# Optimization experiments

Measured on AMD Instinct MI355X. Metric: run time of the kernel, lower is better.

Reference implementation:

```python
import jax, jax.numpy as jnp
import numpy as np

N_NODES = 50000
N_EDGES = 800000


def setup_inputs() -> dict:
    key = jax.random.key(0)
    ks = jax.random.split(key, 8)
    return {
        "x": jax.random.normal(ks[0], (N_NODES, 256), dtype=jnp.float32),
        "adj_vals": jax.random.uniform(ks[1], (N_EDGES,), dtype=jnp.float32),
        "rows": jax.random.randint(ks[2], (N_EDGES,), 0, N_NODES, dtype=jnp.int32),
        "cols": jax.random.randint(ks[3], (N_EDGES,), 0, N_NODES, dtype=jnp.int32),
        "W1": jax.random.normal(ks[4], (256, 256), dtype=jnp.float32) * (1.0 / np.sqrt(256)),
        "b1": jnp.zeros((256,), dtype=jnp.float32),
        "W2": jax.random.normal(ks[5], (256, 256), dtype=jnp.float32) * (1.0 / np.sqrt(256)),
        "b2": jnp.zeros((256,), dtype=jnp.float32),
        "W3": jax.random.normal(ks[6], (256, 128), dtype=jnp.float32) * (1.0 / np.sqrt(256)),
        "b3": jnp.zeros((128,), dtype=jnp.float32),
    }


def reference(x, adj_vals, rows, cols, W1, b1, W2, b2, W3, b3):
    n = x.shape[0]

    def spmm(h):
        # sparse adjacency matmul: out[r] += val * h[c] over all edges (r, c)
        return jax.ops.segment_sum(adj_vals[:, None] * h[cols], rows, num_segments=n)

    # GCNLayer: adj @ (x @ W) + b ; ReLU between layers (dropout p=0 => identity)
    h = jax.nn.relu(spmm(x @ W1) + b1)
    h = jax.nn.relu(spmm(h @ W2) + b2)
    return spmm(h @ W3) + b3
```

## Files before the change

kernel.cpp:

```cpp
#include <hip/hip_runtime.h>
#include <hip/hip_bf16.h>


#define N_NODES 50000
#define N_EDGES 800000
#define KDIM 256
#define REP 8
#define NC (N_NODES * REP)
#define NB2 ((NC + 1023) / 1024)
#define NC_PAD (NB2 * 1024)

typedef __attribute__((ext_vector_type(8))) short short8;
typedef __attribute__((ext_vector_type(4))) float f32x4;

__device__ __forceinline__ ushort f2bf(float f) {
    union { float f; unsigned u; } x; x.f = f;
    unsigned r = x.u + 0x7fffu + ((x.u >> 16) & 1u);
    return (ushort)(r >> 16);
}
__device__ __forceinline__ float bf2f(ushort u) {
    union { unsigned u; float f; } x; x.u = ((unsigned)u) << 16;
    return x.f;
}

__global__ __launch_bounds__(256) void transpose_all_kernel(
        const float* __restrict__ W1, const float* __restrict__ W2,
        const float* __restrict__ W3, ushort* __restrict__ Wt1,
        ushort* __restrict__ Wt2, ushort* __restrict__ Wt3) {
    int id = blockIdx.x * blockDim.x + threadIdx.x;
    if (id < 65536) {
        int n = id >> 8, k = id & 255;
        Wt1[n * 256 + k] = f2bf(W1[k * 256 + n]);
    } else if (id < 131072) {
        int i = id - 65536, n = i >> 8, k = i & 255;
        Wt2[n * 256 + k] = f2bf(W2[k * 256 + n]);
    } else if (id < 163840) {
        int i = id - 131072, n = i >> 8, k = i & 255;
        Wt3[n * 256 + k] = f2bf(W3[k * 128 + n]);
    }
}


#define LDK 40

template <bool AFP32>
__device__ __forceinline__ void gemm_body(
        const void* __restrict__ Ain, const ushort* __restrict__ Wt,
        ushort* __restrict__ C, int M, int N, int bx, int by) {
    __shared__ ushort As[128 * LDK];
    __shared__ ushort Ws[128 * LDK];

    int t = threadIdx.x;
    int lane = t & 63;
    int w = t >> 6;
    int row0 = bx * 128, col0 = by * 128;
    int wm = (w & 1) * 64, wn = (w >> 1) * 64;
    int q = lane >> 4, mi = lane & 15;
    int r0 = t >> 2, kc = (t & 3) * 8;

    f32x4 acc[4][4];
    #pragma unroll
    for (int i = 0; i < 4; i++)
        #pragma unroll
        for (int j = 0; j < 4; j++) acc[i][j] = (f32x4)0.f;

    for (int k0 = 0; k0 < KDIM; k0 += 32) {
        int ga0 = row0 + r0;       if (ga0 >= M) ga0 = M - 1;
        int ga1 = row0 + r0 + 64;  if (ga1 >= M) ga1 = M - 1;
        short8 a0, a1;
        if (AFP32) {
            const float* Af = (const float*)Ain;
            float4 f0 = *(const float4*)&Af[ga0 * KDIM + k0 + kc];
            float4 f1 = *(const float4*)&Af[ga0 * KDIM + k0 + kc + 4];
            float4 f2 = *(const float4*)&Af[ga1 * KDIM + k0 + kc];
            float4 f3 = *(const float4*)&Af[ga1 * KDIM + k0 + kc + 4];
            a0[0] = (short)f2bf(f0.x); a0[1] = (short)f2bf(f0.y);
            a0[2] = (short)f2bf(f0.z); a0[3] = (short)f2bf(f0.w);
            a0[4] = (short)f2bf(f1.x); a0[5] = (short)f2bf(f1.y);
            a0[6] = (short)f2bf(f1.z); a0[7] = (short)f2bf(f1.w);
            a1[0] = (short)f2bf(f2.x); a1[1] = (short)f2bf(f2.y);
            a1[2] = (short)f2bf(f2.z); a1[3] = (short)f2bf(f2.w);
            a1[4] = (short)f2bf(f3.x); a1[5] = (short)f2bf(f3.y);
            a1[6] = (short)f2bf(f3.z); a1[7] = (short)f2bf(f3.w);
        } else {
            const ushort* Ab = (const ushort*)Ain;
            a0 = *(const short8*)&Ab[ga0 * KDIM + k0 + kc];
            a1 = *(const short8*)&Ab[ga1 * KDIM + k0 + kc];
        }
        short8 b0 = *(const short8*)&Wt[(col0 + r0) * KDIM + k0 + kc];
        short8 b1 = *(const short8*)&Wt[(col0 + r0 + 64) * KDIM + k0 + kc];
        __syncthreads();
        *(short8*)&As[r0 * LDK + kc]        = a0;
        *(short8*)&As[(r0 + 64) * LDK + kc] = a1;
        *(short8*)&Ws[r0 * LDK + kc]        = b0;
        *(short8*)&Ws[(r0 + 64) * LDK + kc] = b1;
        __syncthreads();

        short8 af[4], bf[4];
        #pragma unroll
        for (int mt = 0; mt < 4; mt++)
            af[mt] = *(const short8*)&As[(wm + mt * 16 + mi) * LDK + q * 8];
        #pragma unroll
        for (int nt = 0; nt < 4; nt++)
            bf[nt] = *(const short8*)&Ws[(wn + nt * 16 + mi) * LDK + q * 8];
        #pragma unroll
        for (int mt = 0; mt < 4; mt++)
            #pragma unroll
            for (int nt = 0; nt < 4; nt++)
                acc[mt][nt] = __builtin_amdgcn_mfma_f32_16x16x32_bf16(
                    af[mt], bf[nt], acc[mt][nt], 0, 0, 0);
    }

    #pragma unroll
    for (int mt = 0; mt < 4; mt++) {
        #pragma unroll
        for (int r = 0; r < 4; r++) {
            int grow = row0 + wm + mt * 16 + q * 4 + r;
            if (grow < M) {
                #pragma unroll
                for (int nt = 0; nt < 4; nt++) {
                    int gcol = col0 + wn + nt * 16 + mi;
                    C[grow * N + gcol] = f2bf(acc[mt][nt][r]);
                }
            }
        }
    }
}

#define GB1 782

__global__ __launch_bounds__(256) void gemm1_hist_kernel(
        const float* __restrict__ x, const ushort* __restrict__ Wt1,
        ushort* __restrict__ C, const int* __restrict__ rows,
        int* __restrict__ counts) {
    int b = blockIdx.x;
    if (b < GB1) {
        gemm_body<true>(x, Wt1, C, N_NODES, 256, b % 391, b / 391);
    } else {
        int e = (b - GB1) * 256 + threadIdx.x;
        if (e < N_EDGES) {
            int r = rows[e];
            atomicAdd(&counts[(r << 3) | (e & 7)], 1);
        }
    }
}

template <bool AFP32>
__global__ __launch_bounds__(256) void gemm_bf16_kernel(
        const void* __restrict__ Ain, const ushort* __restrict__ Wt,
        ushort* __restrict__ C, int M, int N) {
    gemm_body<AFP32>(Ain, Wt, C, M, N, blockIdx.x, blockIdx.y);
}


__global__ __launch_bounds__(256) void scan_sums(const int* __restrict__ counts,
                                                 int* __restrict__ bsum) {
    __shared__ int ws[4];
    int b = blockIdx.x, t = threadIdx.x, lane = t & 63, wv = t >> 6;
    int4 v = *(const int4*)&counts[b * 1024 + t * 4];
    int s = v.x + v.y + v.z + v.w;
    #pragma unroll
    for (int off = 32; off >= 1; off >>= 1) s += __shfl_down(s, off, 64);
    if (lane == 0) ws[wv] = s;
    __syncthreads();
    if (t == 0) bsum[b] = ws[0] + ws[1] + ws[2] + ws[3];
}

__global__ __launch_bounds__(512) void scan_block(const int* __restrict__ bsum,
                                                  int* __restrict__ boff,
                                                  int* __restrict__ rp8, int nb) {
    __shared__ int ws[8];
    int t = threadIdx.x, lane = t & 63, wv = t >> 6;
    int v = (t < nb) ? bsum[t] : 0;
    int incl = v;
    #pragma unroll
    for (int off = 1; off < 64; off <<= 1) {
        int u = __shfl_up(incl, off, 64);
        if (lane >= off) incl += u;
    }
    if (lane == 63) ws[wv] = incl;
    __syncthreads();
    int wo = 0;
    #pragma unroll
    for (int j = 0; j < 7; j++) wo += (j < wv) ? ws[j] : 0;
    if (t < nb) boff[t] = wo + incl - v;
    if (t == 511) rp8[NC] = wo + incl;
}

__global__ __launch_bounds__(256) void scan_apply(int* __restrict__ counts,
                                                  const int* __restrict__ boff,
                                                  int* __restrict__ rp8) {
    __shared__ int ws[4];
    int b = blockIdx.x, t = threadIdx.x, lane = t & 63, wv = t >> 6;
    int i = b * 1024 + t * 4;
    int4 v = *(const int4*)&counts[i];
    int s0 = v.x, s01 = s0 + v.y, s012 = s01 + v.z, tsum = s012 + v.w;
    int incl = tsum;
    #pragma unroll
    for (int off = 1; off < 64; off <<= 1) {
        int u = __shfl_up(incl, off, 64);
        if (lane >= off) incl += u;
    }
    if (lane == 63) ws[wv] = incl;
    __syncthreads();
    int woff = 0;
    #pragma unroll
    for (int j = 0; j < 3; j++) woff += (j < wv) ? ws[j] : 0;
    int base = boff[b] + woff + incl - tsum;
    if (i < NC)     rp8[i]     = base;
    if (i + 1 < NC) rp8[i + 1] = base + s0;
    if (i + 2 < NC) rp8[i + 2] = base + s01;
    if (i + 3 < NC) rp8[i + 3] = base + s012;
    *(int4*)&counts[i] = make_int4(0, 0, 0, 0);
}

__global__ void scatter_kernel(const int* __restrict__ rows, const int* __restrict__ cols,
                               const float* __restrict__ vals, const int* __restrict__ rp8,
                               int* __restrict__ counts, int2* __restrict__ cv) {
    int e = blockIdx.x * blockDim.x + threadIdx.x;
    if (e < N_EDGES) {
        int idx = (rows[e] << 3) | (e & 7);
        int pos = rp8[idx] + atomicAdd(&counts[idx], 1);
        cv[pos] = make_int2(cols[e], __float_as_int(vals[e]));
    }
}


template <int F, bool RELU, bool OUT_BF16>
__global__ __launch_bounds__(256) void spmm_kernel(
        const ushort* __restrict__ H, const int* __restrict__ rp8,
        const int2* __restrict__ cv, const float* __restrict__ bias,
        void* __restrict__ out, int nrows) {
    constexpr int FL = F / 8;
    constexpr int EP = 64 / FL;
    constexpr int STEP = EP * 4;
    int wave = threadIdx.x >> 6, lane = threadIdx.x & 63;
    int r = blockIdx.x * 4 + wave;
    if (r >= nrows) return;
    int fl = lane % FL, ep = lane / FL;
    const ushort* Hl = H + fl * 8;

    float acc[8];
    #pragma unroll
    for (int j = 0; j < 8; j++) acc[j] = 0.f;

    int start = rp8[r * REP], end = rp8[r * REP + REP];
    for (int base = start; base < end; base += STEP) {
        int e0 = base + ep * 4;
        int2 m0 = cv[e0], m1 = cv[e0 + 1], m2 = cv[e0 + 2], m3 = cv[e0 + 3];
        int   c0 = (e0     < end) ? m0.x : 0;
        int   c1 = (e0 + 1 < end) ? m1.x : 0;
        int   c2 = (e0 + 2 < end) ? m2.x : 0;
        int   c3 = (e0 + 3 < end) ? m3.x : 0;
        float v0 = (e0     < end) ? __int_as_float(m0.y) : 0.f;
        float v1 = (e0 + 1 < end) ? __int_as_float(m1.y) : 0.f;
        float v2 = (e0 + 2 < end) ? __int_as_float(m2.y) : 0.f;
        float v3 = (e0 + 3 < end) ? __int_as_float(m3.y) : 0.f;
        short8 h0 = *(const short8*)&Hl[(size_t)c0 * F];
        short8 h1 = *(const short8*)&Hl[(size_t)c1 * F];
        short8 h2 = *(const short8*)&Hl[(size_t)c2 * F];
        short8 h3 = *(const short8*)&Hl[(size_t)c3 * F];
        #pragma unroll
        for (int j = 0; j < 8; j++)
            acc[j] += v0 * bf2f((ushort)h0[j]) + v1 * bf2f((ushort)h1[j])
                    + v2 * bf2f((ushort)h2[j]) + v3 * bf2f((ushort)h3[j]);
    }

    #pragma unroll
    for (int off = FL; off < 64; off <<= 1)
        #pragma unroll
        for (int j = 0; j < 8; j++) acc[j] += __shfl_down(acc[j], off, 64);

    if (ep == 0) {
        #pragma unroll
        for (int j = 0; j < 8; j++) {
            float o = acc[j] + bias[fl * 8 + j];
            if (RELU) o = fmaxf(o, 0.f);
            acc[j] = o;
        }
        if (OUT_BF16) {
            short8 ob;
            #pragma unroll
            for (int j = 0; j < 8; j++) ob[j] = (short)f2bf(acc[j]);
            *(short8*)((ushort*)out + (size_t)r * F + fl * 8) = ob;
        } else {
            float* of = (float*)out + (size_t)r * F + fl * 8;
            *(float4*)&of[0] = make_float4(acc[0], acc[1], acc[2], acc[3]);
            *(float4*)&of[4] = make_float4(acc[4], acc[5], acc[6], acc[7]);
        }
    }
}


extern "C" void kernel_launch(void* const* d_in, const int* in_sizes, int n_in,
                              void* d_out, int out_size, void* d_ws, size_t ws_size,
                              hipStream_t stream) {
    const float* x    = (const float*)d_in[0];
    const float* av   = (const float*)d_in[1];
    const int*   rows = (const int*)d_in[2];
    const int*   cols = (const int*)d_in[3];
    const float* W1   = (const float*)d_in[4];
    const float* b1   = (const float*)d_in[5];
    const float* W2   = (const float*)d_in[6];
    const float* b2   = (const float*)d_in[7];
    const float* W3   = (const float*)d_in[8];
    const float* b3   = (const float*)d_in[9];
    float* out = (float*)d_out;

    const int N = N_NODES, E = N_EDGES;

    char* p = (char*)d_ws;
    auto carve = [&](size_t bytes) {
        void* q = (void*)p;
        p += (bytes + 255) & ~(size_t)255;
        return q;
    };
    ushort* bufG = (ushort*)carve((size_t)N * 256 * 2);
    ushort* bufH = (ushort*)carve((size_t)N * 256 * 2);
    ushort* Wt1  = (ushort*)carve((size_t)256 * 256 * 2);
    ushort* Wt2  = (ushort*)carve((size_t)256 * 256 * 2);
    ushort* Wt3  = (ushort*)carve((size_t)128 * 256 * 2);
    int*    rp8    = (int*)carve((size_t)(NC + 1) * 4);
    int*    counts = (int*)carve((size_t)NC_PAD * 4);
    int*    bsum   = (int*)carve((size_t)NB2 * 4);
    int*    boff   = (int*)carve((size_t)NB2 * 4);
    int2*   cv     = (int2*)carve((size_t)(E + 16) * 8);

    hipMemsetAsync(counts, 0, (size_t)NC_PAD * 4, stream);
    transpose_all_kernel<<<(163840 + 255) / 256, 256, 0, stream>>>(W1, W2, W3, Wt1, Wt2, Wt3);

    gemm1_hist_kernel<<<GB1 + (E + 255) / 256, 256, 0, stream>>>(x, Wt1, bufG, rows, counts);

    scan_sums<<<NB2, 256, 0, stream>>>(counts, bsum);
    scan_block<<<1, 512, 0, stream>>>(bsum, boff, rp8, NB2);
    scan_apply<<<NB2, 256, 0, stream>>>(counts, boff, rp8);
    scatter_kernel<<<(E + 255) / 256, 256, 0, stream>>>(rows, cols, av, rp8, counts, cv);

    int spmm_blocks = (N + 3) / 4;
    spmm_kernel<256, true, true><<<spmm_blocks, 256, 0, stream>>>(bufG, rp8, cv, b1, bufH, N);
    gemm_bf16_kernel<false><<<dim3(391, 2), 256, 0, stream>>>(bufH, Wt2, bufG, N, 256);
    spmm_kernel<256, true, true><<<spmm_blocks, 256, 0, stream>>>(bufG, rp8, cv, b2, bufH, N);
    gemm_bf16_kernel<false><<<dim3(391, 1), 256, 0, stream>>>(bufH, Wt3, bufG, N, 128);
    spmm_kernel<128, false, false><<<spmm_blocks, 256, 0, stream>>>(bufG, rp8, cv, b3, out, N);
}
```

Measured before the change: 372.6 us.

## Load A fragments directly from global and stage W in half-K LDS chunks

The GEMM body stops staging the A tile through LDS. Each wave now loads its A fragments straight from global memory in MFMA layout. W is staged in two 128-wide K halves using a fragment-ordered LDS layout, which cuts the per-32-K barriers down to two per half. This removes the LDS round trip and most synchronisation for A, but A rows are now read redundantly by the two waves that share rows, and the global loads are less coalesced.

```diff
diff --git a/kernel.cpp b/kernel.cpp
--- a/kernel.cpp
+++ b/kernel.cpp
@@ -41,14 +41,11 @@
 }
 
 
-#define LDK 40
-
 template <bool AFP32>
 __device__ __forceinline__ void gemm_body(
         const void* __restrict__ Ain, const ushort* __restrict__ Wt,
         ushort* __restrict__ C, int M, int N, int bx, int by) {
-    __shared__ ushort As[128 * LDK];
-    __shared__ ushort Ws[128 * LDK];
+    __shared__ ushort Ws[2048 * 8];
 
     int t = threadIdx.x;
     int lane = t & 63;
@@ -56,7 +53,9 @@
     int row0 = bx * 128, col0 = by * 128;
     int wm = (w & 1) * 64, wn = (w >> 1) * 64;
     int q = lane >> 4, mi = lane & 15;
-    int r0 = t >> 2, kc = (t & 3) * 8;
+
+    const ushort* Ab = (const ushort*)Ain;
+    const float*  Af = (const float*)Ain;
 
     f32x4 acc[4][4];
     #pragma unroll
@@ -64,51 +63,50 @@
         #pragma unroll
         for (int j = 0; j < 4; j++) acc[i][j] = (f32x4)0.f;
 
-    for (int k0 = 0; k0 < KDIM; k0 += 32) {
-        int ga0 = row0 + r0;       if (ga0 >= M) ga0 = M - 1;
-        int ga1 = row0 + r0 + 64;  if (ga1 >= M) ga1 = M - 1;
-        short8 a0, a1;
-        if (AFP32) {
-            const float* Af = (const float*)Ain;
-            float4 f0 = *(const float4*)&Af[ga0 * KDIM + k0 + kc];
-            float4 f1 = *(const float4*)&Af[ga0 * KDIM + k0 + kc + 4];
-            float4 f2 = *(const float4*)&Af[ga1 * KDIM + k0 + kc];
-            float4 f3 = *(const float4*)&Af[ga1 * KDIM + k0 + kc + 4];
-            a0[0] = (short)f2bf(f0.x); a0[1] = (short)f2bf(f0.y);
-            a0[2] = (short)f2bf(f0.z); a0[3] = (short)f2bf(f0.w);
-            a0[4] = (short)f2bf(f1.x); a0[5] = (short)f2bf(f1.y);
-            a0[6] = (short)f2bf(f1.z); a0[7] = (short)f2bf(f1.w);
-            a1[0] = (short)f2bf(f2.x); a1[1] = (short)f2bf(f2.y);
-            a1[2] = (short)f2bf(f2.z); a1[3] = (short)f2bf(f2.w);
-            a1[4] = (short)f2bf(f3.x); a1[5] = (short)f2bf(f3.y);
-            a1[6] = (short)f2bf(f3.z); a1[7] = (short)f2bf(f3.w);
-        } else {
-            const ushort* Ab = (const ushort*)Ain;
-            a0 = *(const short8*)&Ab[ga0 * KDIM + k0 + kc];
-            a1 = *(const short8*)&Ab[ga1 * KDIM + k0 + kc];
-        }
-        short8 b0 = *(const short8*)&Wt[(col0 + r0) * KDIM + k0 + kc];
-        short8 b1 = *(const short8*)&Wt[(col0 + r0 + 64) * KDIM + k0 + kc];
+    for (int half = 0; half < 2; half++) {
+        int kbase = half * 128;
+        if (half) __syncthreads();
+        #pragma unroll
+        for (int i = 0; i < 8; i++) {
+            int s = i * 256 + t;
+            int scol = ((s >> 8) << 4) | (s & 15);
+            int sk   = kbase + ((s >> 6) & 3) * 32 + ((s >> 4) & 3) * 8;
+            *(short8*)&Ws[s * 8] =
+                *(const short8*)&Wt[(size_t)(col0 + scol) * KDIM + sk];
+        }
         __syncthreads();
-        *(short8*)&As[r0 * LDK + kc]        = a0;
-        *(short8*)&As[(r0 + 64) * LDK + kc] = a1;
-        *(short8*)&Ws[r0 * LDK + kc]        = b0;
-        *(short8*)&Ws[(r0 + 64) * LDK + kc] = b1;
-        __syncthreads();
-
-        short8 af[4], bf[4];
-        #pragma unroll
-        for (int mt = 0; mt < 4; mt++)
-            af[mt] = *(const short8*)&As[(wm + mt * 16 + mi) * LDK + q * 8];
-        #pragma unroll
-        for (int nt = 0; nt < 4; nt++)
-            bf[nt] = *(const short8*)&Ws[(wn + nt * 16 + mi) * LDK + q * 8];
-        #pragma unroll
-        for (int mt = 0; mt < 4; mt++)
+
+        #pragma unroll
+        for (int kb = 0; kb < 4; kb++) {
+            int k0 = kbase + kb * 32;
+            short8 af[4], bfr[4];
             #pragma unroll
-            for (int nt = 0; nt < 4; nt++)
-                acc[mt][nt] = __builtin_amdgcn_mfma_f32_16x16x32_bf16(
-                    af[mt], bf[nt], acc[mt][nt], 0, 0, 0);
+            for (int mt = 0; mt < 4; mt++) {
+                int ga = row0 + wm + mt * 16 + mi;
+                if (ga >= M) ga = M - 1;
+                if (AFP32) {
+                    float4 f0 = *(const float4*)&Af[(size_t)ga * KDIM + k0 + q * 8];
+                    float4 f1 = *(const float4*)&Af[(size_t)ga * KDIM + k0 + q * 8 + 4];
+                    af[mt][0] = (short)f2bf(f0.x); af[mt][1] = (short)f2bf(f0.y);
+                    af[mt][2] = (short)f2bf(f0.z); af[mt][3] = (short)f2bf(f0.w);
+                    af[mt][4] = (short)f2bf(f1.x); af[mt][5] = (short)f2bf(f1.y);
+                    af[mt][6] = (short)f2bf(f1.z); af[mt][7] = (short)f2bf(f1.w);
+                } else {
+                    af[mt] = *(const short8*)&Ab[(size_t)ga * KDIM + k0 + q * 8];
+                }
+            }
+            #pragma unroll
+            for (int nt = 0; nt < 4; nt++) {
+                int g = (wn >> 4) + nt;
+                bfr[nt] = *(const short8*)&Ws[((g * 4 + kb) * 64 + lane) * 8];
+            }
+            #pragma unroll
+            for (int mt = 0; mt < 4; mt++)
+                #pragma unroll
+                for (int nt = 0; nt < 4; nt++)
+                    acc[mt][nt] = __builtin_amdgcn_mfma_f32_16x16x32_bf16(
+                        af[mt], bfr[nt], acc[mt][nt], 0, 0, 0);
+        }
     }
 
     #pragma unroll
```

New measurement: 394.9 us. 1.06x slower.
